# Optimization experiments

Measured on AMD Instinct MI355X. Metric: run time of the kernel, lower is better.

The kernel has to match this reference:

```python
import jax, jax.numpy as jnp
import numpy as np

N_NODES = 100_000
N_EDGES = 1_600_000
VOCAB = 128
NUM_GRAPHS = 2048


def setup_inputs() -> dict:
    key = jax.random.key(0)
    ks = jax.random.split(key, 8)
    node_ids = jax.random.randint(ks[0], (N_NODES,), 0, VOCAB)
    edge_index = jax.random.randint(ks[1], (2, N_EDGES), 0, N_NODES)
    batch = jnp.sort(jax.random.randint(ks[2], (N_NODES,), 0, NUM_GRAPHS))
    emb = jax.random.normal(ks[3], (VOCAB, 64), jnp.float32) * 0.1
    W1 = jax.random.normal(ks[4], (64, 128), jnp.float32) * (1.0 / np.sqrt(64))
    b1 = jnp.zeros((128,), jnp.float32)
    W2 = jax.random.normal(ks[5], (128, 64), jnp.float32) * (1.0 / np.sqrt(128))
    b2 = jnp.zeros((64,), jnp.float32)
    fc_w = jax.random.normal(ks[6], (1, 64), jnp.float32) * (1.0 / np.sqrt(64))
    fc_b = jnp.zeros((1,), jnp.float32)
    return {"node_ids": node_ids, "edge_index": edge_index, "batch": batch,
            "emb": emb, "W1": W1, "b1": b1, "W2": W2, "b2": b2,
            "fc_w": fc_w, "fc_b": fc_b}


def _gcn_layer(x, W, b, src, dst, norm, n_nodes):
    # x: [N, Fin] -> transform then gather-normalize-scatter (PyG GCNConv)
    h = x @ W                                   # [N, Fout]
    msg = norm[:, None] * h[src]                # [E+N, Fout]
    out = jax.ops.segment_sum(msg, dst, num_segments=n_nodes)
    return out + b


def reference(node_ids, edge_index, batch, emb, W1, b1, W2, b2, fc_w, fc_b):
    n = node_ids.shape[0]
    loop = jnp.arange(n, dtype=edge_index.dtype)
    src = jnp.concatenate([edge_index[0], loop])    # self-loops added (GCNConv default)
    dst = jnp.concatenate([edge_index[1], loop])
    # symmetric normalization: deg^{-1/2}[src] * deg^{-1/2}[dst], deg from dst (in-degree incl. self-loop)
    deg = jax.ops.segment_sum(jnp.ones_like(src, dtype=jnp.float32), dst, num_segments=n)
    dis = jax.lax.rsqrt(jnp.maximum(deg, 1.0))
    norm = dis[src] * dis[dst]

    x = emb[node_ids]                                # [N, 64]
    x = jax.nn.relu(_gcn_layer(x, W1, b1, src, dst, norm, n))
    x = jax.nn.relu(_gcn_layer(x, W2, b2, src, dst, norm, n))

    # global mean pool over graphs
    counts = jax.ops.segment_sum(jnp.ones((n,), jnp.float32), batch, num_segments=NUM_GRAPHS)
    pooled = jax.ops.segment_sum(x, batch, num_segments=NUM_GRAPHS)
    pooled = pooled / jnp.maximum(counts, 1.0)[:, None]   # [G, 64]
    # dropout is identity in eval mode
    logits = pooled @ fc_w.T + fc_b                 # [G, 1]
    return jax.nn.sigmoid(logits).squeeze(-1)       # [G]
```

## Files before the change

### kernel.cpp

```cpp
#include <hip/hip_runtime.h>
#include <math.h>

typedef short short8 __attribute__((ext_vector_type(8)));
typedef float f32x4 __attribute__((ext_vector_type(4)));
typedef float f32x2 __attribute__((ext_vector_type(2)));

#define WP 132
#define OP 136
#define SC_C 8192
#define SC_NB 832
#define GCAP 1024
#define DG_SUB 16
#define DG_LCAP 1024

#if defined(__has_builtin)
#if __has_builtin(__builtin_amdgcn_cvt_pk_f32_fp8) && \
    __has_builtin(__builtin_amdgcn_cvt_pk_fp8_f32)
#define GFP8 1
#endif
#endif
#ifndef GFP8
#define GFP8 0
#endif


__device__ __forceinline__ short f2bf(float x) {
    unsigned u = __float_as_uint(x);
    u += 0x7fffu + ((u >> 16) & 1u);
    return (short)(u >> 16);
}

__global__ void k_cnt_tabs(const int* __restrict__ dst, int* __restrict__ wcnt,
                           const float* __restrict__ emb,
                           const float* __restrict__ W1,
                           const float* __restrict__ W2,
                           short* __restrict__ T1T, short* __restrict__ W2T,
                           int E, int N, int PBLK) {
    if (blockIdx.x >= PBLK) {
        int id = (blockIdx.x - PBLK) * 256 + threadIdx.x;
        if (id < 128 * 128) {
            int f = id >> 7, c = id & 127;
            float acc = 0.f;
#pragma unroll
            for (int k = 0; k < 64; ++k) acc += emb[c * 64 + k] * W1[k * 128 + f];
            T1T[id] = f2bf(acc);
        } else {
            int id2 = id - 128 * 128;
            if (id2 < 64 * 128) {
                int f = id2 >> 7, k = id2 & 127;
                W2T[id2] = f2bf(W2[k * 64 + f]);
            }
        }
        return;
    }
    int lane = threadIdx.x & 63;
    int gw = blockIdx.x * 4 + (threadIdx.x >> 6);
    int TOT = PBLK * 4;
    int cnt[8] = {0, 0, 0, 0, 0, 0, 0, 0};
    for (long long base = (long long)gw * 64; base < E; base += (long long)TOT * 64) {
        int i = (int)base + lane;
        bool valid = (i < E);
        int d = valid ? dst[i] : 0;
        int b = valid ? (int)(((long long)d * 8) / N) : -1;
#pragma unroll
        for (int k = 0; k < 8; ++k)
            cnt[k] += (int)__popcll(__ballot(b == k));
    }
#pragma unroll
    for (int k = 0; k < 8; ++k)
        if (lane == 0) wcnt[k * TOT + gw] = cnt[k];
}

__global__ void k_scat(const int* __restrict__ src, const int* __restrict__ dst,
                       const int* __restrict__ wscan, unsigned* __restrict__ sp1,
                       int E, int N) {
    int lane = threadIdx.x & 63;
    int gw = blockIdx.x * 4 + (threadIdx.x >> 6);
    int TOT = gridDim.x * 4;
    int cur[8];
#pragma unroll
    for (int k = 0; k < 8; ++k) cur[k] = wscan[k * TOT + gw];
    for (long long base = (long long)gw * 64; base < E; base += (long long)TOT * 64) {
        int i = (int)base + lane;
        bool valid = (i < E);
        int d = 0, s = 0;
        if (valid) { d = dst[i]; s = src[i]; }
        int b = valid ? (int)(((long long)d * 8) / N) : -1;
        unsigned packed = 0;
        if (valid) {
            int lo = (int)((long long)N * b / 8);
            packed = ((unsigned)s << 14) | (unsigned)(d - lo);
        }
#pragma unroll
        for (int k = 0; k < 8; ++k) {
            unsigned long long mk = __ballot(b == k);
            if (b == k) {
                int pref = (int)__popcll(mk & ((1ull << lane) - 1ull));
                sp1[cur[k] + pref] = packed;
            }
            cur[k] += (int)__popcll(mk);
        }
    }
}

__global__ __launch_bounds__(1024) void k_deg3(
        const unsigned* __restrict__ sp1, const int* __restrict__ wscan,
        int* __restrict__ degi2, int E, int N, int TOTW) {
    __shared__ int h[DG_LCAP];
    int b   = blockIdx.x & 7;
    int hf  = (blockIdx.x >> 3) & 1;
    int sb  = blockIdx.x >> 4;
    int tid = threadIdx.x;
    int lo = (int)((long long)N * b / 8);
    int hi = (int)((long long)N * (b + 1) / 8);
    int range = hi - lo;
    int sub = (range + DG_SUB - 1) / DG_SUB;
    int nlo = sb * sub;
    int nhi = min(nlo + sub, range);
    int cnt = nhi - nlo;
    if (cnt <= 0) return;
    for (int i = tid; i < cnt; i += 1024) h[i] = 0;
    __syncthreads();
    int beg = wscan[b * TOTW];
    int end = (b < 7) ? wscan[(b + 1) * TOTW] : E;
    int span = end - beg;
    int hb = beg + hf * (span >> 1);
    int he = (hf == 0) ? (beg + (span >> 1)) : end;
    for (int i = hb + tid; i < he; i += 1024) {
        int dl = (int)(sp1[i] & 16383u) - nlo;
        if ((unsigned)dl < (unsigned)cnt) atomicAdd(&h[dl], 1);
    }
    __syncthreads();
    int* dout = degi2 + (size_t)hf * N + lo + nlo;
    for (int i = tid; i < cnt; i += 1024) dout[i] = h[i];
}

__global__ __launch_bounds__(256) void k_scat2(
        const unsigned* __restrict__ sp1, const int* __restrict__ wscan,
        int* __restrict__ tcur, unsigned* __restrict__ sp2,
        int E, int N, int TOTW) {
    __shared__ unsigned staged[SC_C];
    __shared__ int hist[SC_NB], hstart[SC_NB], hoff[SC_NB], gbase[SC_NB];
    __shared__ int sdata[256];
    int b = blockIdx.x & 7;
    int nb = gridDim.x >> 3, bi = blockIdx.x >> 3;
    int lo = (int)((long long)N * b / 8);
    int t0 = lo >> 4;
    int beg = wscan[b * TOTW];
    int end = (b < 7) ? wscan[(b + 1) * TOTW] : E;
    int tid = threadIdx.x;

    for (int cb = beg + bi * SC_C; cb < end; cb += nb * SC_C) {
        int count = min(SC_C, end - cb);
        for (int j = tid; j < SC_NB; j += 256) hist[j] = 0;
        __syncthreads();

        unsigned v[SC_C / 256];
#pragma unroll
        for (int j = 0; j < SC_C / 256; ++j) {
            int i = j * 256 + tid;
            v[j] = 0;
            if (i < count) {
                unsigned sp = sp1[cb + i];
                v[j] = sp;
                int d = (int)(sp & 16383u) + lo;
                atomicAdd(&hist[(d >> 4) - t0], 1);
            }
        }
        __syncthreads();

        int loc[4]; int lsum = 0;
#pragma unroll
        for (int j = 0; j < 4; ++j) {
            int idx = tid * 4 + j;
            loc[j] = (idx < SC_NB) ? hist[idx] : 0;
            lsum += loc[j];
        }
        sdata[tid] = lsum;
        __syncthreads();
        for (int off = 1; off < 256; off <<= 1) {
            int add = (tid >= off) ? sdata[tid - off] : 0;
            __syncthreads();
            sdata[tid] += add;
            __syncthreads();
        }
        int excl = sdata[tid] - lsum;
        int run = 0;
#pragma unroll
        for (int j = 0; j < 4; ++j) {
            int idx = tid * 4 + j;
            if (idx < SC_NB) { hstart[idx] = excl + run; hoff[idx] = excl + run; }
            run += loc[j];
        }
        __syncthreads();

        for (int j = tid; j < SC_NB; j += 256)
            if (hist[j] > 0) gbase[j] = atomicAdd(&tcur[t0 + j], hist[j]);
#pragma unroll
        for (int j = 0; j < SC_C / 256; ++j) {
            int i = j * 256 + tid;
            if (i < count) {
                int d = (int)(v[j] & 16383u) + lo;
                int bin = (d >> 4) - t0;
                int old = atomicAdd(&hoff[bin], 1);
                staged[old] = v[j];
            }
        }
        __syncthreads();

        for (int i = tid; i < count; i += 256) {
            unsigned sp = staged[i];
            int d = (int)(sp & 16383u) + lo;
            int bin = (d >> 4) - t0;
            int pos = gbase[bin] + (i - hstart[bin]);
            unsigned s = sp >> 14;
            sp2[pos] = (s << 4) | (unsigned)(d & 15);
        }
        __syncthreads();
    }
}

__global__ void k_scan_a(const int* __restrict__ in, const int* __restrict__ in2,
                         int* __restrict__ outp, int* __restrict__ csums,
                         float* __restrict__ dis, const int* __restrict__ nid,
                         int2* __restrict__ ndpk, int n) {
    __shared__ int sdata[256];
    int tid = threadIdx.x;
    int idx = blockIdx.x * 1024 + tid * 4;
    int v[4];
#pragma unroll
    for (int j = 0; j < 4; ++j) {
        v[j] = 0;
        if (idx + j < n) {
            v[j] = in[idx + j];
            if (in2 != nullptr) v[j] += in2[idx + j];
            if (dis != nullptr) {
                float dv = rsqrtf((float)(v[j] + 1));
                dis[idx + j] = dv;
                int2 nd; nd.x = nid[idx + j]; nd.y = __float_as_int(dv);
                ndpk[idx + j] = nd;
            }
        }
    }
    int tsum = v[0] + v[1] + v[2] + v[3];
    sdata[tid] = tsum;
    __syncthreads();
    for (int off = 1; off < 256; off <<= 1) {
        int add = (tid >= off) ? sdata[tid - off] : 0;
        __syncthreads();
        sdata[tid] += add;
        __syncthreads();
    }
    int excl = sdata[tid] - tsum;
    int run = 0;
#pragma unroll
    for (int j = 0; j < 4; ++j) {
        if (idx + j < n) outp[idx + j] = excl + run;
        run += v[j];
    }
    if (tid == 255) csums[blockIdx.x] = sdata[255];
}

__global__ void k_scan_b(int* __restrict__ csums, int nch) {
    __shared__ int sdata[256];
    int tid = threadIdx.x;
    int v[4];
#pragma unroll
    for (int j = 0; j < 4; ++j) {
        int i = tid * 4 + j;
        v[j] = (i < nch) ? csums[i] : 0;
    }
    int tsum = v[0] + v[1] + v[2] + v[3];
    sdata[tid] = tsum;
    __syncthreads();
    for (int off = 1; off < 256; off <<= 1) {
        int add = (tid >= off) ? sdata[tid - off] : 0;
        __syncthreads();
        sdata[tid] += add;
        __syncthreads();
    }
    int excl = sdata[tid] - tsum;
    int run = 0;
#pragma unroll
    for (int j = 0; j < 4; ++j) {
        int i = tid * 4 + j;
        if (i < nch) csums[i] = excl + run;
        run += v[j];
    }
}

__global__ void k_scan_c(int* __restrict__ outp, const int* __restrict__ csums,
                         int n, int E, int writeTail, int* __restrict__ tcur) {
    int idx = blockIdx.x * 1024 + threadIdx.x * 4;
    int add = csums[blockIdx.x];
#pragma unroll
    for (int j = 0; j < 4; ++j) {
        int k = idx + j;
        if (k < n) {
            int r = outp[k] + add;
            outp[k] = r;
            if (tcur != nullptr && (k & 15) == 0) tcur[k >> 4] = r;
        }
    }
    if (writeTail && blockIdx.x == 0 && threadIdx.x == 0) outp[n] = E;
}

__global__ __launch_bounds__(256) void k_fused(
        const int* __restrict__ rowptr, const unsigned* __restrict__ sp2,
        const int2* __restrict__ ndpk, const float* __restrict__ dis,
        const short* __restrict__ T1T, const short* __restrict__ W2T,
        const float* __restrict__ b1, void* __restrict__ gq, int N) {
    __shared__ __align__(16) float wtile[16 * WP];
    __shared__ unsigned short otile[16 * OP];
    int tid = threadIdx.x;
    int v0 = blockIdx.x * 16;
    int nloc = min(16, N - v0);

    f32x4* w4 = (f32x4*)wtile;
    for (int i = tid; i < 16 * WP / 4; i += 256) {
        f32x4 z = {0.f, 0.f, 0.f, 0.f};
        w4[i] = z;
    }
    __syncthreads();

    if (tid < nloc) {
        int2 nd = ndpk[v0 + tid];
        atomicAdd(&wtile[tid * WP + nd.x], __int_as_float(nd.y));
    }
    int e0 = rowptr[v0], e1 = rowptr[min(v0 + 16, N)];
    for (int base = e0; base < e1; base += 1024) {
        unsigned sp[4];
        int2 nd[4];
#pragma unroll
        for (int j = 0; j < 4; ++j) {
            int i = base + tid + j * 256;
            sp[j] = (i < e1) ? sp2[i] : 0xffffffffu;
        }
#pragma unroll
        for (int j = 0; j < 4; ++j)
            if (sp[j] != 0xffffffffu) nd[j] = ndpk[sp[j] >> 4];
#pragma unroll
        for (int j = 0; j < 4; ++j)
            if (sp[j] != 0xffffffffu)
                atomicAdd(&wtile[(sp[j] & 15u) * WP + nd[j].x],
                          __int_as_float(nd[j].y));
    }
    __syncthreads();

    int wid = tid >> 6, lane = tid & 63;
    int m = lane & 15, g4 = lane >> 4;

    short8 a[4];
#pragma unroll
    for (int s = 0; s < 4; ++s) {
        float av[8];
        *(f32x4*)(av)     = *(const f32x4*)&wtile[m * WP + g4 * 8 + s * 32];
        *(f32x4*)(av + 4) = *(const f32x4*)&wtile[m * WP + g4 * 8 + s * 32 + 4];
        short8 f;
#pragma unroll
        for (int i = 0; i < 8; ++i) f[i] = f2bf(av[i]);
        a[s] = f;
    }
    float dvals[4];
#pragma unroll
    for (int r = 0; r < 4; ++r) {
        int v = v0 + g4 * 4 + r;
        dvals[r] = (v < N) ? dis[v] : 0.f;
    }

#pragma unroll
    for (int t = 0; t < 2; ++t) {
        int nt = wid * 2 + t;
        f32x4 acc = {0.f, 0.f, 0.f, 0.f};
        const short8* bp = (const short8*)(T1T + (size_t)(nt * 16 + m) * 128 + g4 * 8);
#pragma unroll
        for (int s = 0; s < 4; ++s)
            acc = __builtin_amdgcn_mfma_f32_16x16x32_bf16(a[s], bp[s * 4], acc, 0, 0, 0);
        int col = nt * 16 + m;
        float bb = b1[col];
#pragma unroll
        for (int r = 0; r < 4; ++r) {
            int row = g4 * 4 + r;
            otile[row * OP + col] =
                (unsigned short)f2bf(fmaxf(dvals[r] * acc[r] + bb, 0.f));
        }
    }
    __syncthreads();

    short8 a2[4];
#pragma unroll
    for (int s = 0; s < 4; ++s)
        a2[s] = *(const short8*)&otile[m * OP + g4 * 8 + s * 32];
    {
        int nt2 = wid;
        f32x4 acc = {0.f, 0.f, 0.f, 0.f};
        const short8* bp = (const short8*)(W2T + (size_t)(nt2 * 16 + m) * 128 + g4 * 8);
#pragma unroll
        for (int s = 0; s < 4; ++s)
            acc = __builtin_amdgcn_mfma_f32_16x16x32_bf16(a2[s], bp[s * 4], acc, 0, 0, 0);
#pragma unroll
        for (int r = 0; r < 4; ++r) {
            int row = g4 * 4 + r;
            if (row < nloc) {
                float val = dvals[r] * acc[r];
                size_t off = (size_t)(v0 + row) * 64 + nt2 * 16 + m;
#if GFP8
                int pk = __builtin_amdgcn_cvt_pk_fp8_f32(val, val, 0, false);
                ((unsigned char*)gq)[off] = (unsigned char)pk;
#else
                ((unsigned short*)gq)[off] = (unsigned short)f2bf(val);
#endif
            }
        }
    }
}

__global__ __launch_bounds__(256) void k_gather3(
        const unsigned* __restrict__ sp2, const int* __restrict__ rowptr,
        const void* __restrict__ gq, const float* __restrict__ dis,
        const float* __restrict__ b2, const int* __restrict__ batch,
        float* __restrict__ pooled, int N) {
    __shared__ int lbuf[GCAP];
    __shared__ int lrp[17];
    __shared__ int ncur[16];
    __shared__ int sb[16];
    __shared__ float xt[16][64];
    int tid = threadIdx.x;
    int v0 = blockIdx.x * 16;
    int nloc = min(16, N - v0);
    if (tid < 17) lrp[tid] = rowptr[min(v0 + tid, N)];
    if (tid >= 32 && tid < 48) {
        int r = tid - 32;
        sb[r] = batch[min(v0 + r, N - 1)];
    }
    __syncthreads();
    int e0 = lrp[0], e1 = lrp[nloc];
    int span = e1 - e0;
    bool fits = (span <= GCAP);

    if (fits) {
        if (tid < 16) ncur[tid] = lrp[tid] - e0;
        __syncthreads();
        for (int i = e0 + tid; i < e1; i += 256) {
            unsigned sp = sp2[i];
            int old = atomicAdd(&ncur[sp & 15u], 1);
            lbuf[old] = (int)(sp >> 4);
        }
        __syncthreads();
    }

    int q = tid >> 4, l = tid & 15;
    if (q < nloc) {
        int v = v0 + q;
        f32x4 acc = {0.f, 0.f, 0.f, 0.f};
#if GFP8
        const unsigned* g32 = (const unsigned*)gq;
        {
            unsigned u = g32[(size_t)v * 16 + l];
            f32x2 lo = __builtin_amdgcn_cvt_pk_f32_fp8((int)u, false);
            f32x2 hi = __builtin_amdgcn_cvt_pk_f32_fp8((int)u, true);
            acc[0] = lo[0]; acc[1] = lo[1]; acc[2] = hi[0]; acc[3] = hi[1];
        }
        if (fits) {
            int e = lrp[q] - e0, re = lrp[q + 1] - e0;
            while (e < re) {
                int cnt = re - e;
                unsigned u[8];
#pragma unroll
                for (int j = 0; j < 8; ++j) {
                    int s = lbuf[min(e + j, re - 1)];
                    u[j] = g32[(size_t)s * 16 + l];
                }
#pragma unroll
                for (int j = 0; j < 8; ++j) {
                    float mask = (j < cnt) ? 1.f : 0.f;
                    f32x2 lo = __builtin_amdgcn_cvt_pk_f32_fp8((int)u[j], false);
                    f32x2 hi = __builtin_amdgcn_cvt_pk_f32_fp8((int)u[j], true);
                    acc[0] += mask * lo[0];
                    acc[1] += mask * lo[1];
                    acc[2] += mask * hi[0];
                    acc[3] += mask * hi[1];
                }
                e += 8;
            }
        } else {
            for (int i = e0; i < e1; ++i) {
                unsigned sp = sp2[i];
                if ((int)(sp & 15u) == q) {
                    unsigned u = g32[(size_t)(sp >> 4) * 16 + l];
                    f32x2 lo = __builtin_amdgcn_cvt_pk_f32_fp8((int)u, false);
                    f32x2 hi = __builtin_amdgcn_cvt_pk_f32_fp8((int)u, true);
                    acc[0] += lo[0]; acc[1] += lo[1];
                    acc[2] += hi[0]; acc[3] += hi[1];
                }
            }
        }
#else
        const uint2* g64 = (const uint2*)gq;
        {
            uint2 su = g64[(size_t)v * 16 + l];
            acc[0] = __uint_as_float(su.x << 16);
            acc[1] = __uint_as_float(su.x & 0xffff0000u);
            acc[2] = __uint_as_float(su.y << 16);
            acc[3] = __uint_as_float(su.y & 0xffff0000u);
        }
        if (fits) {
            int e = lrp[q] - e0, re = lrp[q + 1] - e0;
            while (e < re) {
                int cnt = re - e;
                uint2 u[8];
#pragma unroll
                for (int j = 0; j < 8; ++j) {
                    int s = lbuf[min(e + j, re - 1)];
                    u[j] = g64[(size_t)s * 16 + l];
                }
#pragma unroll
                for (int j = 0; j < 8; ++j) {
                    float mask = (j < cnt) ? 1.f : 0.f;
                    acc[0] += mask * __uint_as_float(u[j].x << 16);
                    acc[1] += mask * __uint_as_float(u[j].x & 0xffff0000u);
                    acc[2] += mask * __uint_as_float(u[j].y << 16);
                    acc[3] += mask * __uint_as_float(u[j].y & 0xffff0000u);
                }
                e += 8;
            }
        } else {
            for (int i = e0; i < e1; ++i) {
                unsigned sp = sp2[i];
                if ((int)(sp & 15u) == q) {
                    uint2 u = g64[(size_t)(sp >> 4) * 16 + l];
                    acc[0] += __uint_as_float(u.x << 16);
                    acc[1] += __uint_as_float(u.x & 0xffff0000u);
                    acc[2] += __uint_as_float(u.y << 16);
                    acc[3] += __uint_as_float(u.y & 0xffff0000u);
                }
            }
        }
#endif
        float dv = dis[v];
        f32x4 bb = *(const f32x4*)(b2 + l * 4);
#pragma unroll
        for (int j = 0; j < 4; ++j)
            xt[q][l * 4 + j] = fmaxf(dv * acc[j] + bb[j], 0.f);
    }
    __syncthreads();

    if (tid < 64) {
        float acc = 0.f;
        int bprev = sb[0];
        for (int r = 0; r < nloc; ++r) {
            int b = sb[r];
            if (b != bprev) {
                atomicAdd(&pooled[(size_t)bprev * 64 + tid], acc);
                acc = 0.f;
                bprev = b;
            }
            acc += xt[r][tid];
        }
        atomicAdd(&pooled[(size_t)bprev * 64 + tid], acc);
    }
}

__device__ __forceinline__ int lower_bound(const int* __restrict__ a, int n, int key) {
    int lo = 0, hi = n;
    while (lo < hi) {
        int mid = (lo + hi) >> 1;
        if (a[mid] < key) lo = mid + 1; else hi = mid;
    }
    return lo;
}

__global__ void k_head(const float* __restrict__ pooled, const int* __restrict__ batch,
                       const float* __restrict__ fc_w, const float* __restrict__ fc_b,
                       float* __restrict__ out, int N, int ngraphs) {
    int gi = (blockIdx.x * 256 + threadIdx.x) >> 6;
    int lane = threadIdx.x & 63;
    if (gi >= ngraphs) return;
    int s = lower_bound(batch, N, gi);
    int e = lower_bound(batch, N, gi + 1);
    float c = fmaxf((float)(e - s), 1.0f);
    float a = (pooled[(size_t)gi * 64 + lane] / c) * fc_w[lane];
#pragma unroll
    for (int off = 32; off >= 1; off >>= 1) a += __shfl_down(a, off);
    if (lane == 0) out[gi] = 1.0f / (1.0f + expf(-(a + fc_b[0])));
}

extern "C" void kernel_launch(void* const* d_in, const int* in_sizes, int n_in,
                              void* d_out, int out_size, void* d_ws, size_t ws_size,
                              hipStream_t stream) {
    const int*   nid   = (const int*)d_in[0];
    const int*   eidx  = (const int*)d_in[1];
    const int*   batch = (const int*)d_in[2];
    const float* emb   = (const float*)d_in[3];
    const float* W1    = (const float*)d_in[4];
    const float* b1    = (const float*)d_in[5];
    const float* W2    = (const float*)d_in[6];
    const float* b2    = (const float*)d_in[7];
    const float* fcw   = (const float*)d_in[8];
    const float* fcb   = (const float*)d_in[9];

    const int N = in_sizes[0];
    const int E = in_sizes[1] / 2;
    const int G = out_size;
    const int T = (N + 15) / 16;
    const int* src = eidx;
    const int* dst = eidx + E;

    char* p = (char*)d_ws;
    auto alloc = [&](size_t bytes) {
        char* r = p;
        p += (bytes + 255) & ~(size_t)255;
        return r;
    };
    const int PBLK = 2048;
    const int TOTW = PBLK * 4;
    const int NW   = 8 * TOTW;
    int*      degi2  = (int*)     alloc((size_t)N * 2 * 4);
    float*    dis    = (float*)   alloc((size_t)N * 4);
    int2*     ndpk   = (int2*)    alloc((size_t)N * 8);
    short*    T1T    = (short*)   alloc(128 * 128 * 2);
    short*    W2T    = (short*)   alloc(64 * 128 * 2);
    int*      rowptr = (int*)     alloc((size_t)(N + 1) * 4);
    int*      csums  = (int*)     alloc(4096 * 4);
    int*      wcnt   = (int*)     alloc((size_t)NW * 4);
    int*      wscan  = (int*)     alloc((size_t)(NW + 1) * 4);
    int*      csums2 = (int*)     alloc(256 * 4);
    int*      tcur   = (int*)     alloc((size_t)(T + 1) * 4);
    unsigned* sp1    = (unsigned*)alloc((size_t)E * 4);
    unsigned* sp2    = (unsigned*)alloc((size_t)E * 4);
    void*     g      = (void*)    alloc((size_t)N * 64 * 2);
    float*    pooled = (float*)   alloc((size_t)G * 64 * 4);

    hipMemsetAsync(pooled, 0, (size_t)G * 64 * 4, stream);

    k_cnt_tabs<<<PBLK + 96, 256, 0, stream>>>(dst, wcnt, emb, W1, W2, T1T, W2T,
                                              E, N, PBLK);

    int nch2 = (NW + 1023) / 1024;
    k_scan_a<<<nch2, 256, 0, stream>>>(wcnt, nullptr, wscan, csums2,
                                       nullptr, nullptr, nullptr, NW);
    k_scan_b<<<1, 256, 0, stream>>>(csums2, nch2);
    k_scan_c<<<nch2, 256, 0, stream>>>(wscan, csums2, NW, 0, 0, nullptr);

    k_scat<<<PBLK, 256, 0, stream>>>(src, dst, wscan, sp1, E, N);
    k_deg3<<<8 * DG_SUB * 2, 1024, 0, stream>>>(sp1, wscan, degi2, E, N, TOTW);

    int nch = (N + 1023) / 1024;
    k_scan_a<<<nch, 256, 0, stream>>>(degi2, degi2 + N, rowptr, csums,
                                      dis, nid, ndpk, N);
    k_scan_b<<<1, 256, 0, stream>>>(csums, nch);
    k_scan_c<<<nch, 256, 0, stream>>>(rowptr, csums, N, E, 1, tcur);

    k_scat2<<<2048, 256, 0, stream>>>(sp1, wscan, tcur, sp2, E, N, TOTW);

    k_fused<<<T, 256, 0, stream>>>(rowptr, sp2, ndpk, dis, T1T, W2T, b1, g, N);

    k_gather3<<<T, 256, 0, stream>>>(sp2, rowptr, g, dis, b2, batch, pooled, N);

    k_head<<<((long long)G * 64 + 255) / 256, 256, 0, stream>>>(
        pooled, batch, fcw, fcb, (float*)d_out, N, G);
}
```

Measured before the change: 166.7 us.

## Fuse edge count and scatter into one kernel with atomic bucket reservation

Merges the per-wave counting kernel, the three-kernel prefix scan over wave counts, and the bucket scatter into one kernel. Each block counts its contiguous edge chunk, reserves space per destination bucket with a global atomicAdd, then scatters into fixed-capacity bucket regions. This removes four launches and the wave-count scan, at the cost of nondeterministic ordering within buckets and a fixed capacity per bucket that could overflow on skewed inputs. k_scat2 also gains an odd extra pass of atomicAdd-zero into the histogram, followed by a re-clear, which adds wasted shared-memory atomics and barriers.

```diff
diff --git a/kernel.cpp b/kernel.cpp
--- a/kernel.cpp
+++ b/kernel.cpp
@@ -30,12 +30,13 @@
     return (short)(u >> 16);
 }
 
-__global__ void k_cnt_tabs(const int* __restrict__ dst, int* __restrict__ wcnt,
-                           const float* __restrict__ emb,
-                           const float* __restrict__ W1,
-                           const float* __restrict__ W2,
-                           short* __restrict__ T1T, short* __restrict__ W2T,
-                           int E, int N, int PBLK) {
+__global__ void k_part_tabs(const int* __restrict__ src, const int* __restrict__ dst,
+                            int* __restrict__ bcur, unsigned* __restrict__ sp1,
+                            const float* __restrict__ emb,
+                            const float* __restrict__ W1,
+                            const float* __restrict__ W2,
+                            short* __restrict__ T1T, short* __restrict__ W2T,
+                            int E, int N, int PBLK, int CAP) {
     if (blockIdx.x >= PBLK) {
         int id = (blockIdx.x - PBLK) * 256 + threadIdx.x;
         if (id < 128 * 128) {
@@ -53,36 +54,48 @@
         }
         return;
     }
-    int lane = threadIdx.x & 63;
-    int gw = blockIdx.x * 4 + (threadIdx.x >> 6);
-    int TOT = PBLK * 4;
+    __shared__ int wcnts[4][8];
+    __shared__ int gbase[8];
+    int tid = threadIdx.x, w = tid >> 6, lane = tid & 63;
+    int CHB = (E + PBLK - 1) / PBLK;
+    int CHW = (CHB + 3) / 4;
+    int bbeg = blockIdx.x * CHB;
+    int bend = min(bbeg + CHB, E);
+    int wbeg = min(bbeg + w * CHW, bend);
+    int wend = min(wbeg + CHW, bend);
+
     int cnt[8] = {0, 0, 0, 0, 0, 0, 0, 0};
-    for (long long base = (long long)gw * 64; base < E; base += (long long)TOT * 64) {
-        int i = (int)base + lane;
-        bool valid = (i < E);
+    for (int base = wbeg; base < wend; base += 64) {
+        int i = base + lane;
+        bool valid = (i < wend);
         int d = valid ? dst[i] : 0;
         int b = valid ? (int)(((long long)d * 8) / N) : -1;
 #pragma unroll
         for (int k = 0; k < 8; ++k)
             cnt[k] += (int)__popcll(__ballot(b == k));
     }
-#pragma unroll
-    for (int k = 0; k < 8; ++k)
-        if (lane == 0) wcnt[k * TOT + gw] = cnt[k];
-}
-
-__global__ void k_scat(const int* __restrict__ src, const int* __restrict__ dst,
-                       const int* __restrict__ wscan, unsigned* __restrict__ sp1,
-                       int E, int N) {
-    int lane = threadIdx.x & 63;
-    int gw = blockIdx.x * 4 + (threadIdx.x >> 6);
-    int TOT = gridDim.x * 4;
-    int cur[8];
-#pragma unroll
-    for (int k = 0; k < 8; ++k) cur[k] = wscan[k * TOT + gw];
-    for (long long base = (long long)gw * 64; base < E; base += (long long)TOT * 64) {
-        int i = (int)base + lane;
-        bool valid = (i < E);
+    if (lane == 0) {
+#pragma unroll
+        for (int k = 0; k < 8; ++k) wcnts[w][k] = cnt[k];
+    }
+    __syncthreads();
+    if (tid < 8) {
+        int tot = wcnts[0][tid] + wcnts[1][tid] + wcnts[2][tid] + wcnts[3][tid];
+        gbase[tid] = (tot > 0) ? atomicAdd(&bcur[tid * 16], tot) : 0;
+    }
+    __syncthreads();
+    int wb[8];
+#pragma unroll
+    for (int k = 0; k < 8; ++k) {
+        int off = gbase[k];
+        if (w > 0) off += wcnts[0][k];
+        if (w > 1) off += wcnts[1][k];
+        if (w > 2) off += wcnts[2][k];
+        wb[k] = off;
+    }
+    for (int base = wbeg; base < wend; base += 64) {
+        int i = base + lane;
+        bool valid = (i < wend);
         int d = 0, s = 0;
         if (valid) { d = dst[i]; s = src[i]; }
         int b = valid ? (int)(((long long)d * 8) / N) : -1;
@@ -96,16 +109,16 @@
             unsigned long long mk = __ballot(b == k);
             if (b == k) {
                 int pref = (int)__popcll(mk & ((1ull << lane) - 1ull));
-                sp1[cur[k] + pref] = packed;
-            }
-            cur[k] += (int)__popcll(mk);
+                sp1[(size_t)k * CAP + wb[k] + pref] = packed;
+            }
+            wb[k] += (int)__popcll(mk);
         }
     }
 }
 
 __global__ __launch_bounds__(1024) void k_deg3(
-        const unsigned* __restrict__ sp1, const int* __restrict__ wscan,
-        int* __restrict__ degi2, int E, int N, int TOTW) {
+        const unsigned* __restrict__ sp1, const int* __restrict__ bcur,
+        int* __restrict__ degi2, int N, int CAP) {
     __shared__ int h[DG_LCAP];
     int b   = blockIdx.x & 7;
     int hf  = (blockIdx.x >> 3) & 1;
@@ -121,13 +134,12 @@
     if (cnt <= 0) return;
     for (int i = tid; i < cnt; i += 1024) h[i] = 0;
     __syncthreads();
-    int beg = wscan[b * TOTW];
-    int end = (b < 7) ? wscan[(b + 1) * TOTW] : E;
-    int span = end - beg;
-    int hb = beg + hf * (span >> 1);
-    int he = (hf == 0) ? (beg + (span >> 1)) : end;
+    int span = bcur[b * 16];
+    const unsigned* pb = sp1 + (size_t)b * CAP;
+    int hb = hf * (span >> 1);
+    int he = (hf == 0) ? (span >> 1) : span;
     for (int i = hb + tid; i < he; i += 1024) {
-        int dl = (int)(sp1[i] & 16383u) - nlo;
+        int dl = (int)(pb[i] & 16383u) - nlo;
         if ((unsigned)dl < (unsigned)cnt) atomicAdd(&h[dl], 1);
     }
     __syncthreads();
@@ -136,9 +148,9 @@
 }
 
 __global__ __launch_bounds__(256) void k_scat2(
-        const unsigned* __restrict__ sp1, const int* __restrict__ wscan,
+        const unsigned* __restrict__ sp1, const int* __restrict__ bcur,
         int* __restrict__ tcur, unsigned* __restrict__ sp2,
-        int E, int N, int TOTW) {
+        int N, int CAP) {
     __shared__ unsigned staged[SC_C];
     __shared__ int hist[SC_NB], hstart[SC_NB], hoff[SC_NB], gbase[SC_NB];
     __shared__ int sdata[256];
@@ -146,11 +158,11 @@
     int nb = gridDim.x >> 3, bi = blockIdx.x >> 3;
     int lo = (int)((long long)N * b / 8);
     int t0 = lo >> 4;
-    int beg = wscan[b * TOTW];
-    int end = (b < 7) ? wscan[(b + 1) * TOTW] : E;
+    int end = bcur[b * 16];
+    const unsigned* pb = sp1 + (size_t)b * CAP;
     int tid = threadIdx.x;
 
-    for (int cb = beg + bi * SC_C; cb < end; cb += nb * SC_C) {
+    for (int cb = bi * SC_C; cb < end; cb += nb * SC_C) {
         int count = min(SC_C, end - cb);
         for (int j = tid; j < SC_NB; j += 256) hist[j] = 0;
         __syncthreads();
@@ -161,9 +173,19 @@
             int i = j * 256 + tid;
             v[j] = 0;
             if (i < count) {
-                unsigned sp = sp1[cb + i];
+                unsigned sp = pb[cb + i];
                 v[j] = sp;
-                int d = (int)(sp & 16383u) + lo;
+                atomicAdd(&hist[(int)(sp & 16383u) >> 4 << 0 ? ((int)((sp & 16383u)) + lo >> 4) - t0 : 0], 0);
+            }
+        }
+        __syncthreads();
+        for (int j = tid; j < SC_NB; j += 256) hist[j] = 0;
+        __syncthreads();
+#pragma unroll
+        for (int j = 0; j < SC_C / 256; ++j) {
+            int i = j * 256 + tid;
+            if (i < count) {
+                int d = (int)(v[j] & 16383u) + lo;
                 atomicAdd(&hist[(d >> 4) - t0], 1);
             }
         }
@@ -613,8 +635,7 @@
         return r;
     };
     const int PBLK = 2048;
-    const int TOTW = PBLK * 4;
-    const int NW   = 8 * TOTW;
+    const int CAP  = E / 8 + E / 32 + 4096;
     int*      degi2  = (int*)     alloc((size_t)N * 2 * 4);
     float*    dis    = (float*)   alloc((size_t)N * 4);
     int2*     ndpk   = (int2*)    alloc((size_t)N * 8);
@@ -622,28 +643,21 @@
     short*    W2T    = (short*)   alloc(64 * 128 * 2);
     int*      rowptr = (int*)     alloc((size_t)(N + 1) * 4);
     int*      csums  = (int*)     alloc(4096 * 4);
-    int*      wcnt   = (int*)     alloc((size_t)NW * 4);
-    int*      wscan  = (int*)     alloc((size_t)(NW + 1) * 4);
-    int*      csums2 = (int*)     alloc(256 * 4);
+    int*      bcur   = (int*)     alloc(8 * 16 * 4);
     int*      tcur   = (int*)     alloc((size_t)(T + 1) * 4);
-    unsigned* sp1    = (unsigned*)alloc((size_t)E * 4);
+    unsigned* sp1    = (unsigned*)alloc((size_t)8 * CAP * 4);
     unsigned* sp2    = (unsigned*)alloc((size_t)E * 4);
     void*     g      = (void*)    alloc((size_t)N * 64 * 2);
     float*    pooled = (float*)   alloc((size_t)G * 64 * 4);
 
     hipMemsetAsync(pooled, 0, (size_t)G * 64 * 4, stream);
-
-    k_cnt_tabs<<<PBLK + 96, 256, 0, stream>>>(dst, wcnt, emb, W1, W2, T1T, W2T,
-                                              E, N, PBLK);
-
-    int nch2 = (NW + 1023) / 1024;
-    k_scan_a<<<nch2, 256, 0, stream>>>(wcnt, nullptr, wscan, csums2,
-                                       nullptr, nullptr, nullptr, NW);
-    k_scan_b<<<1, 256, 0, stream>>>(csums2, nch2);
-    k_scan_c<<<nch2, 256, 0, stream>>>(wscan, csums2, NW, 0, 0, nullptr);
-
-    k_scat<<<PBLK, 256, 0, stream>>>(src, dst, wscan, sp1, E, N);
-    k_deg3<<<8 * DG_SUB * 2, 1024, 0, stream>>>(sp1, wscan, degi2, E, N, TOTW);
+    hipMemsetAsync(bcur, 0, 8 * 16 * 4, stream);
+
+    k_part_tabs<<<PBLK + 96, 256, 0, stream>>>(src, dst, bcur, sp1,
+                                               emb, W1, W2, T1T, W2T,
+                                               E, N, PBLK, CAP);
+
+    k_deg3<<<8 * DG_SUB * 2, 1024, 0, stream>>>(sp1, bcur, degi2, N, CAP);
 
     int nch = (N + 1023) / 1024;
     k_scan_a<<<nch, 256, 0, stream>>>(degi2, degi2 + N, rowptr, csums,
@@ -651,7 +665,7 @@
     k_scan_b<<<1, 256, 0, stream>>>(csums, nch);
     k_scan_c<<<nch, 256, 0, stream>>>(rowptr, csums, N, E, 1, tcur);
 
-    k_scat2<<<2048, 256, 0, stream>>>(sp1, wscan, tcur, sp2, E, N, TOTW);
+    k_scat2<<<2048, 256, 0, stream>>>(sp1, bcur, tcur, sp2, N, CAP);
 
     k_fused<<<T, 256, 0, stream>>>(rowptr, sp2, ndpk, dis, T1T, W2T, b1, g, N);
 
```

Measured after the change: 200.4 us. 20.3% more time.
